# Optimization experiments

Hardware: AMD Instinct MI355X
Metric: run time of the kernel (lower is better)

Reference implementation:

```python
import jax, jax.numpy as jnp
import numpy as np

D_IN = 1024
D_OUT = 1024

def setup_inputs() -> dict:
    key = jax.random.key(0)
    kx, kq, kk, kv = jax.random.split(key, 4)
    x = jax.random.normal(kx, (4, 2048, D_IN), dtype=jnp.float32)
    # torch Linear weights are [d_out, d_in]; store as [d_in, d_out] for x @ W
    s = 1.0 / np.sqrt(D_IN)
    Wq = jax.random.uniform(kq, (D_IN, D_OUT), jnp.float32, -s, s)
    Wk = jax.random.uniform(kk, (D_IN, D_OUT), jnp.float32, -s, s)
    Wv = jax.random.uniform(kv, (D_IN, D_OUT), jnp.float32, -s, s)
    return {"x": x, "Wq": Wq, "Wk": Wk, "Wv": Wv}

def reference(x, Wq, Wk, Wv):
    # x: [b, n, d_in]
    n = x.shape[1]
    q = jnp.einsum('bnd,de->bne', x, Wq)
    k = jnp.einsum('bnd,de->bne', x, Wk)
    v = jnp.einsum('bnd,de->bne', x, Wv)
    scores = jnp.einsum('bqe,bke->bqk', q, k)  # [b, n, n]
    causal = jnp.tril(jnp.ones((n, n), dtype=bool))  # True = keep
    scores = jnp.where(causal, scores, -jnp.inf)
    attn = jax.nn.softmax(scores / jnp.sqrt(jnp.float32(k.shape[-1])), axis=-1)
    # dropout p=0.0 -> identity
    return jnp.einsum('bqk,bke->bqe', attn, v)
```

## Files before the change

### kernel.cpp

```cpp
#include <hip/hip_runtime.h>
#include <hip/hip_bf16.h>
#include <stdint.h>

#define D_ 1024
#define NSEQ 2048

typedef __attribute__((ext_vector_type(8))) short bf16x8;
typedef __attribute__((ext_vector_type(4))) float f32x4;

static __device__ __forceinline__ unsigned short f2bf(float x) {
    union { __hip_bfloat16 h; unsigned short u; } cv;
    cv.h = __float2bfloat16(x);
    return cv.u;
}

static __device__ __forceinline__ void gload_lds16(const void* g, void* l) {
    __builtin_amdgcn_global_load_lds(
        (const __attribute__((address_space(1))) unsigned int*)(uintptr_t)g,
        (__attribute__((address_space(3))) unsigned int*)(uintptr_t)l, 16, 0, 0);
}

__global__ __launch_bounds__(256) void prep(const float* __restrict__ x,
                                            const float* __restrict__ Wq,
                                            const float* __restrict__ Wk,
                                            const float* __restrict__ Wv,
                                            __hip_bfloat16* __restrict__ xb,
                                            __hip_bfloat16* __restrict__ Wt) {
    __shared__ float tile[32][33];
    const int b = blockIdx.x;
    const int t = threadIdx.x;
    if (b < 8192) {
        int i = b * 256 + t;
        float4 v = reinterpret_cast<const float4*>(x)[i];
        ushort4 o;
        o.x = f2bf(v.x); o.y = f2bf(v.y); o.z = f2bf(v.z); o.w = f2bf(v.w);
        reinterpret_cast<ushort4*>(xb)[i] = o;
        return;
    }
    const int b2 = b - 8192;
    const int z = b2 >> 10, rem = b2 & 1023;
    const int cx = rem & 31, cy = rem >> 5;
    const float* W = (z == 0) ? Wq : (z == 1) ? Wk : Wv;
    unsigned short* O = (unsigned short*)(Wt + (size_t)z * D_ * D_);
    int r0 = cy * 32, c0 = cx * 32;
    int r = t >> 3, c4 = (t & 7) * 4;
    float4 v = *reinterpret_cast<const float4*>(&W[(size_t)(r0 + r) * D_ + c0 + c4]);
    tile[r][c4 + 0] = v.x; tile[r][c4 + 1] = v.y;
    tile[r][c4 + 2] = v.z; tile[r][c4 + 3] = v.w;
    __syncthreads();
    int er = t >> 3, dc = (t & 7) * 4;
    ushort4 pk;
    pk.x = f2bf(tile[dc + 0][er]); pk.y = f2bf(tile[dc + 1][er]);
    pk.z = f2bf(tile[dc + 2][er]); pk.w = f2bf(tile[dc + 3][er]);
    *reinterpret_cast<ushort4*>(&O[(size_t)(c0 + er) * D_ + r0 + dc]) = pk;
}

__global__ __launch_bounds__(512) void gemm_qkv(
    const __hip_bfloat16* __restrict__ A,
    const __hip_bfloat16* __restrict__ Bt,
    void* __restrict__ q_out, void* __restrict__ k_out, void* __restrict__ vt_out) {
    constexpr int NT = 16;

    __shared__ __hip_bfloat16 As[256 * 64];
    __shared__ __hip_bfloat16 Bs[128 * 64];

    const int m0 = blockIdx.x * 256, n0 = blockIdx.y * 128;
    const int tid = threadIdx.x, lane = tid & 63, wid = tid >> 6;
    const int wm = wid >> 1, wn = wid & 1;
    const int lr = lane & 15, lk = lane >> 4;

    const __hip_bfloat16* Apan = A + (size_t)m0 * 1024;
    const __hip_bfloat16* Bpan = Bt + (size_t)n0 * 1024;

    const __hip_bfloat16* asrc[4];
    const __hip_bfloat16* bsrc[2];
#pragma unroll
    for (int r = 0; r < 4; ++r) {
        const int c = (wid * 4 + r) * 64 + lane;
        const int row = c >> 3, slot = c & 7;
        asrc[r] = Apan + (size_t)row * 1024 + (slot ^ (row & 7)) * 8;
    }
#pragma unroll
    for (int r = 0; r < 2; ++r) {
        const int c = (wid * 2 + r) * 64 + lane;
        const int row = c >> 3, slot = c & 7;
        bsrc[r] = Bpan + (size_t)row * 1024 + (slot ^ (row & 7)) * 8;
    }

    const int sw = lr & 7;
    const int slot0 = (lk ^ sw) * 16, slot1 = ((4 + lk) ^ sw) * 16;

    f32x4 acc[4][4] = {};

    for (int t = 0; t < NT; ++t) {
#pragma unroll
        for (int r = 0; r < 4; ++r) {
            gload_lds16(asrc[r], (char*)As + (wid * 4 + r) * 1024);
            asrc[r] += 64;
        }
#pragma unroll
        for (int r = 0; r < 2; ++r) {
            gload_lds16(bsrc[r], (char*)Bs + (wid * 2 + r) * 1024);
            bsrc[r] += 64;
        }
        __syncthreads();

        bf16x8 af0[4], af1[4], bf0[4], bf1[4];
#pragma unroll
        for (int m = 0; m < 4; ++m) {
            const int ra = (wm * 64 + m * 16 + lr) * 128;
            const int rb = (wn * 64 + m * 16 + lr) * 128;
            af0[m] = *reinterpret_cast<const bf16x8*>((const char*)As + ra + slot0);
            af1[m] = *reinterpret_cast<const bf16x8*>((const char*)As + ra + slot1);
            bf0[m] = *reinterpret_cast<const bf16x8*>((const char*)Bs + rb + slot0);
            bf1[m] = *reinterpret_cast<const bf16x8*>((const char*)Bs + rb + slot1);
        }
        __builtin_amdgcn_s_setprio(1);
#pragma unroll
        for (int m = 0; m < 4; ++m)
#pragma unroll
            for (int n = 0; n < 4; ++n)
                acc[m][n] = __builtin_amdgcn_mfma_f32_16x16x32_bf16(af0[m], bf0[n], acc[m][n], 0, 0, 0);
#pragma unroll
        for (int m = 0; m < 4; ++m)
#pragma unroll
            for (int n = 0; n < 4; ++n)
                acc[m][n] = __builtin_amdgcn_mfma_f32_16x16x32_bf16(af1[m], bf1[n], acc[m][n], 0, 0, 0);
        __builtin_amdgcn_s_setprio(0);
        __syncthreads();
    }

#pragma unroll
    for (int m = 0; m < 4; ++m)
#pragma unroll
        for (int n = 0; n < 4; ++n) {
            const int rbase = m0 + wm * 64 + m * 16 + lk * 4;
            const int cbase = n0 + wn * 64 + n * 16 + lr;
            const int seg = cbase >> 10, e = cbase & 1023;
            if (seg < 2) {
                unsigned short* C = (unsigned short*)(seg == 0 ? q_out : k_out);
#pragma unroll
                for (int j = 0; j < 4; ++j)
                    C[(size_t)(rbase + j) * D_ + e] = f2bf(acc[m][n][j]);
            } else {
                unsigned short* Vt = (unsigned short*)vt_out;
                const int b = rbase >> 11, nq = rbase & 2047;
                ushort4 pk;
                pk.x = f2bf(acc[m][n][0]); pk.y = f2bf(acc[m][n][1]);
                pk.z = f2bf(acc[m][n][2]); pk.w = f2bf(acc[m][n][3]);
                *reinterpret_cast<ushort4*>(&Vt[(((size_t)b << 10) + e) * NSEQ + nq]) = pk;
            }
        }
}

template <int MODE>
__global__ __launch_bounds__(256) void gemm128(const __hip_bfloat16* __restrict__ A, int lda,
                                               const __hip_bfloat16* __restrict__ Bt, int ldb,
                                               void* __restrict__ o0, void* __restrict__ o1,
                                               const float* __restrict__ rinv) {
    int bx, by, bz;
    if (MODE == 2) {
        const int fid = blockIdx.x;
        bz = fid & 3;
        const int t = fid >> 2;
        bx = (int)((sqrtf(8.0f * t + 1.0f) - 1.0f) * 0.5f);
        while ((bx + 1) * (bx + 2) / 2 <= t) ++bx;
        while (bx * (bx + 1) / 2 > t) --bx;
        by = t - bx * (bx + 1) / 2;
    } else {
        const int fid = blockIdx.x;
        const int bxr = fid & 15;
        bx = (fid & 256) ? 15 - bxr : bxr;
        bz = (fid >> 4) & 3;
        by = fid >> 6;
    }

    const __hip_bfloat16* Ab = A;
    const __hip_bfloat16* Bb = Bt;
    int Kdim = 1024;
    if (MODE == 2) { Ab += (size_t)bz * NSEQ * lda; Bb += (size_t)bz * NSEQ * ldb; }
    if (MODE == 3) { Ab += (size_t)bz * NSEQ * lda; Bb += (size_t)bz * D_ * ldb; Kdim = (bx + 1) * 128; }

    const int m0 = bx * 128, n0 = by * 128;

    __shared__ __hip_bfloat16 As[128 * 64];
    __shared__ __hip_bfloat16 Bs[128 * 64];

    const int tid = threadIdx.x;
    const int lane = tid & 63, wid = tid >> 6;
    const int wm = wid >> 1, wn = wid & 1;
    const int lr = lane & 15, lk = lane >> 4;

    const __hip_bfloat16* asrc[4];
    const __hip_bfloat16* bsrc[4];
#pragma unroll
    for (int r = 0; r < 4; ++r) {
        const int chunk = r * 256 + tid;
        const int row = chunk >> 3, slot = chunk & 7;
        const int col = ((slot ^ (row & 7)) * 8);
        asrc[r] = Ab + (size_t)(m0 + row) * lda + col;
        bsrc[r] = Bb + (size_t)(n0 + row) * ldb + col;
    }

    const int sw = lr & 7;
    const int slotA0 = (lk ^ sw) * 16, slotA1 = ((4 + lk) ^ sw) * 16;

    f32x4 acc[4][4] = {};

    for (int k0 = 0; k0 < Kdim; k0 += 64) {
#pragma unroll
        for (int r = 0; r < 4; ++r) {
            gload_lds16(asrc[r], (char*)As + r * 4096 + wid * 1024);
            gload_lds16(bsrc[r], (char*)Bs + r * 4096 + wid * 1024);
            asrc[r] += 64; bsrc[r] += 64;
        }
        __syncthreads();

        bf16x8 af0[4], bf0[4], af1[4], bf1[4];
#pragma unroll
        for (int m = 0; m < 4; ++m) {
            const int ra = (wm * 64 + m * 16 + lr) * 128;
            const int rb = (wn * 64 + m * 16 + lr) * 128;
            af0[m] = *reinterpret_cast<const bf16x8*>((const char*)As + ra + slotA0);
            af1[m] = *reinterpret_cast<const bf16x8*>((const char*)As + ra + slotA1);
            bf0[m] = *reinterpret_cast<const bf16x8*>((const char*)Bs + rb + slotA0);
            bf1[m] = *reinterpret_cast<const bf16x8*>((const char*)Bs + rb + slotA1);
        }
#pragma unroll
        for (int m = 0; m < 4; ++m)
#pragma unroll
            for (int n = 0; n < 4; ++n)
                acc[m][n] = __builtin_amdgcn_mfma_f32_16x16x32_bf16(af0[m], bf0[n], acc[m][n], 0, 0, 0);
#pragma unroll
        for (int m = 0; m < 4; ++m)
#pragma unroll
            for (int n = 0; n < 4; ++n)
                acc[m][n] = __builtin_amdgcn_mfma_f32_16x16x32_bf16(af1[m], bf1[n], acc[m][n], 0, 0, 0);
        __syncthreads();
    }

    if (MODE == 2) {
        unsigned short* P = (unsigned short*)o0 + (size_t)bz * NSEQ * NSEQ;
#pragma unroll
        for (int m = 0; m < 4; ++m)
#pragma unroll
            for (int n = 0; n < 4; ++n) {
                const int rbase = m0 + wm * 64 + m * 16 + lk * 4;
                const int cbase = n0 + wn * 64 + n * 16 + lr;
#pragma unroll
                for (int j = 0; j < 4; ++j) {
                    float p = (cbase > rbase + j) ? 0.0f
                              : __expf(acc[m][n][j] * 0.03125f);
                    acc[m][n][j] = p;
                    P[(size_t)(rbase + j) * NSEQ + cbase] = f2bf(p);
                }
            }
        float* Pl = (float*)o1;
        const int pcol = by * 2 + wn;
#pragma unroll
        for (int m = 0; m < 4; ++m)
#pragma unroll
            for (int j = 0; j < 4; ++j) {
                float sm = (acc[m][0][j] + acc[m][1][j]) + (acc[m][2][j] + acc[m][3][j]);
#pragma unroll
                for (int w = 1; w < 16; w <<= 1) sm += __shfl_xor(sm, w, 64);
                if (lr == 0) {
                    const int row = bz * NSEQ + m0 + wm * 64 + m * 16 + lk * 4 + j;
                    Pl[row * 32 + pcol] = sm;
                }
            }
    } else {
        float* O = (float*)o0 + (size_t)bz * NSEQ * D_;
#pragma unroll
        for (int m = 0; m < 4; ++m)
#pragma unroll
            for (int n = 0; n < 4; ++n) {
                const int rbase = m0 + wm * 64 + m * 16 + lk * 4;
                const int cbase = n0 + wn * 64 + n * 16 + lr;
#pragma unroll
                for (int j = 0; j < 4; ++j)
                    O[(size_t)(rbase + j) * D_ + cbase] =
                        acc[m][n][j] * rinv[bz * NSEQ + rbase + j];
            }
    }
}

__global__ __launch_bounds__(256) void sum_merge(const float* __restrict__ Pl,
                                                 float* __restrict__ rinv) {
    int row = blockIdx.x * 256 + threadIdx.x;
    int q = row & 2047;
    int nc = 2 * ((q >> 7) + 1);
    float l = 0.f;
    for (int c = 0; c < nc; ++c) l += Pl[row * 32 + c];
    rinv[row] = 1.0f / l;
}

extern "C" void kernel_launch(void* const* d_in, const int* in_sizes, int n_in,
                              void* d_out, int out_size, void* d_ws, size_t ws_size,
                              hipStream_t stream) {
    const float* x  = (const float*)d_in[0];
    const float* Wq = (const float*)d_in[1];
    const float* Wk = (const float*)d_in[2];
    const float* Wv = (const float*)d_in[3];

    char* ws = (char*)d_ws;
    unsigned short* P    = (unsigned short*)(ws);
    __hip_bfloat16* Xb   = (__hip_bfloat16*)(ws + 67108864);
    __hip_bfloat16* Q    = (__hip_bfloat16*)(ws + 83886080);
    __hip_bfloat16* K    = (__hip_bfloat16*)(ws + 100663296);
    __hip_bfloat16* Vt   = (__hip_bfloat16*)(ws + 117440512);
    __hip_bfloat16* Wt   = (__hip_bfloat16*)(ws + 134217728);
    float*  Pl = (float*)(ws + 67108864);
    float*  rl = (float*)(ws + 69206016);

    prep<<<11264, 256, 0, stream>>>(x, Wq, Wk, Wv, Xb, Wt);

    gemm_qkv<<<dim3(32, 24), 512, 0, stream>>>(Xb, Wt, Q, K, Vt);

    gemm128<2><<<dim3(544), 256, 0, stream>>>(Q, 1024, K, 1024, P, Pl, nullptr);
    sum_merge<<<32, 256, 0, stream>>>(Pl, rl);
    gemm128<3><<<dim3(512), 256, 0, stream>>>((const __hip_bfloat16*)P, 2048, Vt, 2048,
                                              d_out, nullptr, rl);
}
```

Baseline: 177.1 us.

## Pipeline QKV GEMM with 4-stage LDS ring and 256x256 tiles

Restructures the QKV projection GEMM to use 256x256 output tiles with K steps of 32, held in a 4-buffer dynamic-LDS ring (128 KB). Loads for three stages ahead are issued with global_load_lds, and explicit vmcnt waits replace the two __syncthreads per step with a single barrier. The goal is to overlap global loads with MFMA work and raise arithmetic intensity per block. In exchange the grid drops to 384 blocks, which fills the CUs unevenly, and the large LDS footprint limits how many blocks can run on a CU at once.

```diff
diff --git a/kernel.cpp b/kernel.cpp
--- a/kernel.cpp
+++ b/kernel.cpp
@@ -55,86 +55,84 @@
     *reinterpret_cast<ushort4*>(&O[(size_t)(c0 + er) * D_ + r0 + dc]) = pk;
 }
 
-__global__ __launch_bounds__(512) void gemm_qkv(
+__global__ __launch_bounds__(512, 2) void gemm_qkv(
     const __hip_bfloat16* __restrict__ A,
     const __hip_bfloat16* __restrict__ Bt,
     void* __restrict__ q_out, void* __restrict__ k_out, void* __restrict__ vt_out) {
-    constexpr int NT = 16;
-
-    __shared__ __hip_bfloat16 As[256 * 64];
-    __shared__ __hip_bfloat16 Bs[128 * 64];
-
-    const int m0 = blockIdx.x * 256, n0 = blockIdx.y * 128;
+    constexpr int NT = 32;
+    extern __shared__ char lds[];
+
+    const int m0 = blockIdx.x * 256, n0 = blockIdx.y * 256;
     const int tid = threadIdx.x, lane = tid & 63, wid = tid >> 6;
-    const int wm = wid >> 1, wn = wid & 1;
+    const int wm = wid >> 2, wn = wid & 3;
     const int lr = lane & 15, lk = lane >> 4;
 
     const __hip_bfloat16* Apan = A + (size_t)m0 * 1024;
     const __hip_bfloat16* Bpan = Bt + (size_t)n0 * 1024;
 
-    const __hip_bfloat16* asrc[4];
+    const __hip_bfloat16* asrc[2];
     const __hip_bfloat16* bsrc[2];
 #pragma unroll
-    for (int r = 0; r < 4; ++r) {
-        const int c = (wid * 4 + r) * 64 + lane;
-        const int row = c >> 3, slot = c & 7;
-        asrc[r] = Apan + (size_t)row * 1024 + (slot ^ (row & 7)) * 8;
-    }
-#pragma unroll
     for (int r = 0; r < 2; ++r) {
-        const int c = (wid * 2 + r) * 64 + lane;
-        const int row = c >> 3, slot = c & 7;
-        bsrc[r] = Bpan + (size_t)row * 1024 + (slot ^ (row & 7)) * 8;
-    }
-
-    const int sw = lr & 7;
-    const int slot0 = (lk ^ sw) * 16, slot1 = ((4 + lk) ^ sw) * 16;
-
-    f32x4 acc[4][4] = {};
+        const int c = wid * 2 + r;
+        const int row = c * 16 + (lane >> 2);
+        const int col = ((lane & 3) ^ ((lane >> 3) & 3)) * 8;
+        asrc[r] = Apan + (size_t)row * 1024 + col;
+        bsrc[r] = Bpan + (size_t)row * 1024 + col;
+    }
+
+    auto stage = [&](int s) {
+        char* base = lds + (s & 3) * 32768;
+#pragma unroll
+        for (int r = 0; r < 2; ++r) {
+            gload_lds16(asrc[r], base + (wid * 2 + r) * 1024);
+            asrc[r] += 32;
+        }
+#pragma unroll
+        for (int r = 0; r < 2; ++r) {
+            gload_lds16(bsrc[r], base + 16384 + (wid * 2 + r) * 1024);
+            bsrc[r] += 32;
+        }
+    };
+
+    const int sw = (lr >> 1) & 3;
+    const int slot0 = (lk ^ sw) * 16;
+
+    f32x4 acc[8][4] = {};
+
+    stage(0); stage(1); stage(2);
 
     for (int t = 0; t < NT; ++t) {
-#pragma unroll
-        for (int r = 0; r < 4; ++r) {
-            gload_lds16(asrc[r], (char*)As + (wid * 4 + r) * 1024);
-            asrc[r] += 64;
-        }
-#pragma unroll
-        for (int r = 0; r < 2; ++r) {
-            gload_lds16(bsrc[r], (char*)Bs + (wid * 2 + r) * 1024);
-            bsrc[r] += 64;
-        }
-        __syncthreads();
-
-        bf16x8 af0[4], af1[4], bf0[4], bf1[4];
-#pragma unroll
-        for (int m = 0; m < 4; ++m) {
-            const int ra = (wm * 64 + m * 16 + lr) * 128;
-            const int rb = (wn * 64 + m * 16 + lr) * 128;
-            af0[m] = *reinterpret_cast<const bf16x8*>((const char*)As + ra + slot0);
-            af1[m] = *reinterpret_cast<const bf16x8*>((const char*)As + ra + slot1);
-            bf0[m] = *reinterpret_cast<const bf16x8*>((const char*)Bs + rb + slot0);
-            bf1[m] = *reinterpret_cast<const bf16x8*>((const char*)Bs + rb + slot1);
-        }
+        if (t < NT - 2)       asm volatile("s_waitcnt vmcnt(8)" ::: "memory");
+        else if (t == NT - 2) asm volatile("s_waitcnt vmcnt(4)" ::: "memory");
+        else                  asm volatile("s_waitcnt vmcnt(0)" ::: "memory");
+        __builtin_amdgcn_s_barrier();
+        if (t + 3 < NT) stage(t + 3);
+
+        const char* Ab = lds + (t & 3) * 32768;
+        const char* Bb = Ab + 16384;
+        bf16x8 af[8], bf[4];
+#pragma unroll
+        for (int m = 0; m < 8; ++m)
+            af[m] = *reinterpret_cast<const bf16x8*>(Ab + (wm * 128 + m * 16 + lr) * 64 + slot0);
+#pragma unroll
+        for (int n = 0; n < 4; ++n)
+            bf[n] = *reinterpret_cast<const bf16x8*>(Bb + (wn * 64 + n * 16 + lr) * 64 + slot0);
+
         __builtin_amdgcn_s_setprio(1);
 #pragma unroll
-        for (int m = 0; m < 4; ++m)
+        for (int m = 0; m < 8; ++m)
 #pragma unroll
             for (int n = 0; n < 4; ++n)
-                acc[m][n] = __builtin_amdgcn_mfma_f32_16x16x32_bf16(af0[m], bf0[n], acc[m][n], 0, 0, 0);
-#pragma unroll
-        for (int m = 0; m < 4; ++m)
-#pragma unroll
-            for (int n = 0; n < 4; ++n)
-                acc[m][n] = __builtin_amdgcn_mfma_f32_16x16x32_bf16(af1[m], bf1[n], acc[m][n], 0, 0, 0);
+                acc[m][n] = __builtin_amdgcn_mfma_f32_16x16x32_bf16(af[m], bf[n], acc[m][n], 0, 0, 0);
         __builtin_amdgcn_s_setprio(0);
-        __syncthreads();
-    }
-
-#pragma unroll
-    for (int m = 0; m < 4; ++m)
+    }
+
+#pragma unroll
+    for (int m = 0; m < 8; ++m)
 #pragma unroll
         for (int n = 0; n < 4; ++n) {
-            const int rbase = m0 + wm * 64 + m * 16 + lk * 4;
+            const int rbase = m0 + wm * 128 + m * 16 + lk * 4;
             const int cbase = n0 + wn * 64 + n * 16 + lr;
             const int seg = cbase >> 10, e = cbase & 1023;
             if (seg < 2) {
@@ -315,7 +313,7 @@
 
     prep<<<11264, 256, 0, stream>>>(x, Wq, Wk, Wv, Xb, Wt);
 
-    gemm_qkv<<<dim3(32, 24), 512, 0, stream>>>(Xb, Wt, Q, K, Vt);
+    gemm_qkv<<<dim3(32, 12), 512, 131072, stream>>>(Xb, Wt, Q, K, Vt);
 
     gemm128<2><<<dim3(544), 256, 0, stream>>>(Q, 1024, K, 1024, P, Pl, nullptr);
     sum_merge<<<32, 256, 0, stream>>>(Pl, rl);
```

Result: faster. 169.6 us (-4.2%).
